# Kernel tuning notes

Measured on AMD Instinct MI355X. Metric: run time of the kernel, lower is better.

## Reference

```python
import jax, jax.numpy as jnp
import numpy as np

N_WIN = 8      # windows per side (j = i = n_win)
NUM_HEADS = 8
TOPK = 4


def setup_inputs() -> dict:
    key = jax.random.key(0)
    k1, k2 = jax.random.split(key)
    cv_feature = jax.random.normal(k1, (1, 128, 128, 256), dtype=jnp.float32)
    mv_feature = jax.random.normal(k2, (1, 4, 128, 128, 256), dtype=jnp.float32)
    return {"cv_feature": cv_feature, "mv_feature": mv_feature}


def reference(cv_feature, mv_feature):
    n, H, W, C = cv_feature.shape
    v = mv_feature.shape[1]
    j = i = N_WIN
    h, w = H // j, W // i
    p2, w2 = j * i, h * w
    m = NUM_HEADS
    ch = C // m
    scale = C ** (-0.5)  # module uses d_model**-0.5 for both routing and pixel attn

    # window partition: n (j h)(i w) c -> n (j i) h w c
    cv_patch = cv_feature.reshape(n, j, h, i, w, C).transpose(0, 1, 3, 2, 4, 5).reshape(n, p2, h, w, C)
    mv_patch = mv_feature.reshape(n, v, j, h, i, w, C).transpose(0, 1, 2, 4, 3, 5, 6).reshape(n, v, p2, h, w, C)

    q_pix = cv_patch.reshape(n, p2, w2, C)          # n p2 w2 c
    kv_pix = mv_patch.reshape(n, v, p2, w2, C)      # n v p2 w2 c

    # window-level pooled queries/keys (routing is detached in the original)
    q_win = jax.lax.stop_gradient(cv_patch.mean((2, 3)))            # n p2 c
    k_win = jax.lax.stop_gradient(mv_patch.mean((3, 4)))            # n v p2 c
    k_win = k_win.reshape(n, v * p2, C)

    logits = jnp.einsum('npc,nqc->npq', q_win * scale, k_win)       # n p2 (v p2)
    topk_logit, r_idx = jax.lax.top_k(logits, TOPK)                 # n p2 k
    r_weight = jax.nn.softmax(topk_logit, axis=-1)                  # computed, unused (faithful)

    # gather routed KV windows: n p2 k w2 c
    kv_flat = kv_pix.reshape(n, v * p2, w2, C)
    kv_sel = jnp.take_along_axis(kv_flat[:, None], r_idx[:, :, :, None, None], axis=2)

    # split heads
    k_sel = kv_sel.reshape(n, p2, TOPK, w2, m, ch)                  # n p2 k w2 m ch
    q = q_pix.reshape(n, p2, w2, m, ch)                             # n p2 w2 m ch

    attn = jnp.einsum('npqmc,npkwmc->npmqkw', q * scale, k_sel)
    attn = attn.reshape(n, p2, m, w2, TOPK * w2)
    attn = jax.nn.softmax(attn, axis=-1)

    v_sel = k_sel.transpose(0, 1, 4, 2, 3, 5).reshape(n, p2, m, TOPK * w2, ch)
    out = jnp.einsum('npmqt,npmtc->npmqc', attn, v_sel)             # n p2 m w2 ch

    # merge heads + window un-partition: -> n H W C
    out = out.transpose(0, 1, 3, 2, 4).reshape(n, j, i, h, w, C)
    out = out.transpose(0, 1, 3, 2, 4, 5).reshape(n, H, W, C)
    return out
```

## Files before the change

kernel.cpp:

```cpp
#include <hip/hip_runtime.h>
#include <hip/hip_bf16.h>


typedef __attribute__((ext_vector_type(4))) float f32x4;
typedef __attribute__((ext_vector_type(8))) short s16x8;
typedef __attribute__((ext_vector_type(4))) short s16x4;
typedef __attribute__((ext_vector_type(2))) unsigned u32x2;
typedef __attribute__((ext_vector_type(4))) unsigned u32x4;

#define SCALE 0.0625f
#define LOG2E 1.44269504088896340736f

__device__ inline unsigned cvt_pk_bf16(float lo, float hi) {
  unsigned r;
  asm("v_cvt_pk_bf16_f32 %0, %1, %2" : "=v"(r) : "v"(lo), "v"(hi));
  return r;
}
__device__ inline unsigned pk_bf16_rne(float lo, float hi) {
  unsigned a = __float_as_uint(lo);
  unsigned b = __float_as_uint(hi);
  a += 0x7FFFu + ((a >> 16) & 1u);
  b += 0x7FFFu + ((b >> 16) & 1u);
  return (a >> 16) | (b & 0xFFFF0000u);
}
#if __has_builtin(__builtin_amdgcn_exp2f)
#define EXP2(x) __builtin_amdgcn_exp2f(x)
#else
#define EXP2(x) exp2f(x)
#endif

__global__ __launch_bounds__(256) void k_means(const float* __restrict__ cv,
                                               const float* __restrict__ mv,
                                               float* __restrict__ qwin,
                                               float* __restrict__ kwin) {
  __shared__ float sm[4][64];
  int wi = blockIdx.x >> 2, cq = blockIdx.x & 3;
  int pq = threadIdx.x >> 6, cl = threadIdx.x & 63;
  int c = cq * 64 + cl;
  const float* base;
  float* dst;
  if (wi < 64) {
    base = cv + ((size_t)((wi >> 3) * 16) * 128 + (wi & 7) * 16) * 256;
    dst = qwin + wi * 256;
  } else {
    int r = wi - 64;
    base = mv + (size_t)(r >> 6) * (128 * 128 * 256)
         + ((size_t)(((r >> 3) & 7) * 16) * 128 + (r & 7) * 16) * 256;
    dst = kwin + r * 256;
  }
  float s = 0.f;
  for (int k = 0; k < 64; ++k) {
    int px = pq * 64 + k;
    s += base[((px >> 4) * 128 + (px & 15)) * 256 + c];
  }
  sm[pq][cl] = s;
  __syncthreads();
  if (pq == 0)
    dst[c] = (sm[0][cl] + sm[1][cl] + sm[2][cl] + sm[3][cl]) * (1.f / 256.f);
}

__global__ __launch_bounds__(256) void k_route(const float* __restrict__ qwin,
                                               const float* __restrict__ kwin,
                                               int* __restrict__ ridx) {
  __shared__ float qrow[256];
  __shared__ float sv[256];
  __shared__ float wbv[4];
  __shared__ int wbi[4];
  int p = blockIdx.x, t = threadIdx.x;
  qrow[t] = qwin[p * 256 + t] * SCALE;
  __syncthreads();
  const f32x4* kr = reinterpret_cast<const f32x4*>(kwin + t * 256);
  float dot = 0.f;
#pragma unroll 4
  for (int c4 = 0; c4 < 64; ++c4) {
    f32x4 kv = kr[c4];
    dot += qrow[c4 * 4 + 0] * kv[0] + qrow[c4 * 4 + 1] * kv[1]
         + qrow[c4 * 4 + 2] * kv[2] + qrow[c4 * 4 + 3] * kv[3];
  }
  sv[t] = dot;
  __syncthreads();
  for (int k = 0; k < 4; ++k) {
    float v = sv[t];
    int ii = t;
#pragma unroll
    for (int off = 32; off > 0; off >>= 1) {
      float ov = __shfl_down(v, off, 64);
      int oi = __shfl_down(ii, off, 64);
      if (ov > v || (ov == v && oi < ii)) { v = ov; ii = oi; }
    }
    if ((t & 63) == 0) { wbv[t >> 6] = v; wbi[t >> 6] = ii; }
    __syncthreads();
    if (t == 0) {
      float bv = wbv[0]; int bi = wbi[0];
      for (int j = 1; j < 4; ++j)
        if (wbv[j] > bv || (wbv[j] == bv && wbi[j] < bi)) { bv = wbv[j]; bi = wbi[j]; }
      ridx[p * 4 + k] = bi;
      sv[bi] = -3.0e38f;
    }
    __syncthreads();
  }
}

__global__ __launch_bounds__(256, 2) void k_attn(const float* __restrict__ cv,
                                                 const float* __restrict__ mv,
                                                 const int* __restrict__ ridx,
                                                 float* __restrict__ out) {
  __shared__ __align__(16) short kv_lds[256 * 32];

  const int tid = threadIdx.x;
  const int lane = tid & 63, wv = tid >> 6;
  const int g = lane >> 4, c16 = lane & 15;
  const int p = blockIdx.x >> 3, m = blockIdx.x & 7;
  const int py = p >> 3, px = p & 7;

  const int4 ridx4 = *reinterpret_cast<const int4*>(ridx + p * 4);

  const float qs = SCALE * LOG2E;
  s16x8 qf[4];
#pragma unroll
  for (int qt = 0; qt < 4; ++qt) {
    const float* qp = cv + ((size_t)((py * 16 + wv * 4 + qt) * 128) + px * 16 + c16) * 256
                         + m * 32 + g * 8;
    f32x4 a = *reinterpret_cast<const f32x4*>(qp);
    f32x4 b = *reinterpret_cast<const f32x4*>(qp + 4);
    union { u32x4 u; s16x8 s; } cu;
    cu.u[0] = cvt_pk_bf16(a[0] * qs, a[1] * qs);
    cu.u[1] = cvt_pk_bf16(a[2] * qs, a[3] * qs);
    cu.u[2] = cvt_pk_bf16(b[0] * qs, b[1] * qs);
    cu.u[3] = cvt_pk_bf16(b[2] * qs, b[3] * qs);
    qf[qt] = cu.s;
  }

  f32x4 accO[4][2];
  float lsum[4];
#pragma unroll
  for (int qt = 0; qt < 4; ++qt) {
    lsum[qt] = 0.f;
    accO[qt][0] = f32x4{0.f, 0.f, 0.f, 0.f};
    accO[qt][1] = f32x4{0.f, 0.f, 0.f, 0.f};
  }
  const f32x4 zf = {0.f, 0.f, 0.f, 0.f};

  for (int w = 0; w < 4; ++w) {
    if (w) __syncthreads();
    {
      int r = (&ridx4.x)[w];
      const float* srcb = mv + (size_t)(r >> 6) * (128 * 128 * 256)
                        + ((size_t)(((r >> 3) & 7) * 16) * 128 + (r & 7) * 16) * 256 + m * 32;
#pragma unroll
      for (int i = 0; i < 8; ++i) {
        int u = i * 256 + tid;
        int pxl = u >> 3, quad = u & 7;
        f32x4 d = *reinterpret_cast<const f32x4*>(
            srcb + ((pxl >> 4) * 128 + (pxl & 15)) * 256 + quad * 4);
        u32x2 pk;
        pk[0] = cvt_pk_bf16(d[0], d[1]);
        pk[1] = cvt_pk_bf16(d[2], d[3]);
        int off = (pxl >> 2) * 128 + (quad >> 2) * 64 + (pxl & 3) * 16 + (quad & 3) * 4;
        *reinterpret_cast<u32x2*>(&kv_lds[off]) = pk;
      }
    }
    __syncthreads();

    for (int s = 0; s < 8; ++s) {
      int kr0 = s * 32 + c16;
      int kr1 = kr0 + 16;
      const s16x8 kf0 = *reinterpret_cast<const s16x8*>(
          &kv_lds[(kr0 >> 2) * 128 + (g >> 1) * 64 + (kr0 & 3) * 16 + (g & 1) * 8]);
      const s16x8 kf1 = *reinterpret_cast<const s16x8*>(
          &kv_lds[(kr1 >> 2) * 128 + (g >> 1) * 64 + (kr1 & 3) * 16 + (g & 1) * 8]);
      s16x8 V0, V1;
#pragma unroll
      for (int j = 0; j < 8; ++j) {
        int a = (s * 8 + (j >> 2) * 4 + g) * 128 + (j & 3) * 16 + c16;
        V0[j] = kv_lds[a];
        V1[j] = kv_lds[a + 64];
      }
#pragma unroll
      for (int qt = 0; qt < 4; ++qt) {
        f32x4 sx = __builtin_amdgcn_mfma_f32_16x16x32_bf16(kf0, qf[qt], zf, 0, 0, 0);
        f32x4 sy = __builtin_amdgcn_mfma_f32_16x16x32_bf16(kf1, qf[qt], zf, 0, 0, 0);
        float x0 = EXP2(sx[0]), x1 = EXP2(sx[1]), x2 = EXP2(sx[2]), x3 = EXP2(sx[3]);
        float y0 = EXP2(sy[0]), y1 = EXP2(sy[1]), y2 = EXP2(sy[2]), y3 = EXP2(sy[3]);
        lsum[qt] += ((x0 + x1) + (x2 + x3)) + ((y0 + y1) + (y2 + y3));
        union { u32x4 u; s16x8 s; } pb;
        pb.u[0] = pk_bf16_rne(x0, x1);
        pb.u[1] = pk_bf16_rne(x2, x3);
        pb.u[2] = pk_bf16_rne(y0, y1);
        pb.u[3] = pk_bf16_rne(y2, y3);
        accO[qt][0] = __builtin_amdgcn_mfma_f32_16x16x32_bf16(V0, pb.s, accO[qt][0], 0, 0, 0);
        accO[qt][1] = __builtin_amdgcn_mfma_f32_16x16x32_bf16(V1, pb.s, accO[qt][1], 0, 0, 0);
      }
    }
  }

#pragma unroll
  for (int qt = 0; qt < 4; ++qt) {
    float l = lsum[qt];
    l += __shfl_xor(l, 16, 64);
    l += __shfl_xor(l, 32, 64);
    float rl = 1.f / l;
#pragma unroll
    for (int mt = 0; mt < 2; ++mt) {
      f32x4 o = accO[qt][mt];
      o[0] *= rl; o[1] *= rl; o[2] *= rl; o[3] *= rl;
      float* op = out + ((size_t)((py * 16 + wv * 4 + qt) * 128) + px * 16 + c16) * 256
                      + m * 32 + mt * 16 + g * 4;
      *reinterpret_cast<f32x4*>(op) = o;
    }
  }
}

extern "C" void kernel_launch(void* const* d_in, const int* in_sizes, int n_in,
                              void* d_out, int out_size, void* d_ws, size_t ws_size,
                              hipStream_t stream) {
  const float* cv = (const float*)d_in[0];
  const float* mv = (const float*)d_in[1];
  float* out = (float*)d_out;

  float* qwin = (float*)d_ws;
  float* kwin = qwin + 64 * 256;
  int* ridx = (int*)(kwin + 256 * 256);

  k_means<<<1280, 256, 0, stream>>>(cv, mv, qwin, kwin);
  k_route<<<64, 256, 0, stream>>>(qwin, kwin, ridx);
  k_attn<<<512, 256, 0, stream>>>(cv, mv, ridx, out);
}
```

Measured before the change: 71.77 us.

## Split attention over routed windows into two partial blocks plus merge kernel

Attention over the four routed KV windows is split across two blocks, each handling two windows, which doubles the grid to 1024 blocks and raises occupancy. Each block writes unnormalised partial outputs and row sums to workspace, and a new merge kernel adds the halves and normalises. This is meant to raise parallelism and latency hiding on a 256-CU device. In exchange it adds roughly 32MB of fp32 partial-output traffic plus an extra launch. If the workspace is too small it falls back to the fused kernel.

Measured after the change: 80.04 us. 11.5% more time.

```diff
diff --git a/kernel.cpp b/kernel.cpp
--- a/kernel.cpp
+++ b/kernel.cpp
@@ -4,7 +4,6 @@
 
 typedef __attribute__((ext_vector_type(4))) float f32x4;
 typedef __attribute__((ext_vector_type(8))) short s16x8;
-typedef __attribute__((ext_vector_type(4))) short s16x4;
 typedef __attribute__((ext_vector_type(2))) unsigned u32x2;
 typedef __attribute__((ext_vector_type(4))) unsigned u32x4;
 
@@ -101,19 +100,16 @@
   }
 }
 
-__global__ __launch_bounds__(256, 2) void k_attn(const float* __restrict__ cv,
-                                                 const float* __restrict__ mv,
-                                                 const int* __restrict__ ridx,
-                                                 float* __restrict__ out) {
-  __shared__ __align__(16) short kv_lds[256 * 32];
-
-  const int tid = threadIdx.x;
-  const int lane = tid & 63, wv = tid >> 6;
+template <int NW>
+__device__ __forceinline__ void attn_core(const float* __restrict__ cv,
+                                          const float* __restrict__ mv,
+                                          const int* __restrict__ rwin,
+                                          short* kv_lds,
+                                          int p, int m, int wv, int lane,
+                                          f32x4 accO[4][2], float lsum[4]) {
   const int g = lane >> 4, c16 = lane & 15;
-  const int p = blockIdx.x >> 3, m = blockIdx.x & 7;
   const int py = p >> 3, px = p & 7;
-
-  const int4 ridx4 = *reinterpret_cast<const int4*>(ridx + p * 4);
+  const int tid = wv * 64 + lane;
 
   const float qs = SCALE * LOG2E;
   s16x8 qf[4];
@@ -131,8 +127,6 @@
     qf[qt] = cu.s;
   }
 
-  f32x4 accO[4][2];
-  float lsum[4];
 #pragma unroll
   for (int qt = 0; qt < 4; ++qt) {
     lsum[qt] = 0.f;
@@ -141,10 +135,10 @@
   }
   const f32x4 zf = {0.f, 0.f, 0.f, 0.f};
 
-  for (int w = 0; w < 4; ++w) {
+  for (int w = 0; w < NW; ++w) {
     if (w) __syncthreads();
     {
-      int r = (&ridx4.x)[w];
+      int r = rwin[w];
       const float* srcb = mv + (size_t)(r >> 6) * (128 * 128 * 256)
                         + ((size_t)(((r >> 3) & 7) * 16) * 128 + (r & 7) * 16) * 256 + m * 32;
 #pragma unroll
@@ -193,6 +187,82 @@
       }
     }
   }
+}
+
+__global__ __launch_bounds__(256, 4) void k_attn_partial(const float* __restrict__ cv,
+                                                         const float* __restrict__ mv,
+                                                         const int* __restrict__ ridx,
+                                                         float* __restrict__ opart,
+                                                         float* __restrict__ lpart) {
+  __shared__ __align__(16) short kv_lds[256 * 32];
+  const int tid = threadIdx.x;
+  const int lane = tid & 63, wv = tid >> 6;
+  const int g = lane >> 4, c16 = lane & 15;
+  const int bid = blockIdx.x;
+  const int half = bid & 1, m = (bid >> 1) & 7, p = bid >> 4;
+
+  int rwin[2];
+  rwin[0] = ridx[p * 4 + half * 2 + 0];
+  rwin[1] = ridx[p * 4 + half * 2 + 1];
+
+  f32x4 accO[4][2];
+  float lsum[4];
+  attn_core<2>(cv, mv, rwin, kv_lds, p, m, wv, lane, accO, lsum);
+
+  float* Ob = opart + ((size_t)(half * 512 + p * 8 + m) * 256) * 32;
+  float* lb = lpart + (size_t)(half * 512 + p * 8 + m) * 256;
+#pragma unroll
+  for (int qt = 0; qt < 4; ++qt) {
+    float l = lsum[qt];
+    l += __shfl_xor(l, 16, 64);
+    l += __shfl_xor(l, 32, 64);
+    int q = (wv * 4 + qt) * 16 + c16;
+    if (g == 0) lb[q] = l;
+#pragma unroll
+    for (int mt = 0; mt < 2; ++mt)
+      *reinterpret_cast<f32x4*>(&Ob[q * 32 + mt * 16 + g * 4]) = accO[qt][mt];
+  }
+}
+
+__global__ __launch_bounds__(256) void k_merge(const float* __restrict__ opart,
+                                               const float* __restrict__ lpart,
+                                               float* __restrict__ out) {
+  int uidx = blockIdx.x * 256 + threadIdx.x;
+  int c4 = uidx & 63;
+  int X = (uidx >> 6) & 127;
+  int Y = uidx >> 13;
+  int p = (Y >> 4) * 8 + (X >> 4);
+  int q = (Y & 15) * 16 + (X & 15);
+  int m = c4 >> 3, ch4 = c4 & 7;
+  size_t pidx = (size_t)(p * 8 + m) * 256 + q;
+  const size_t HSTRIDE = (size_t)512 * 256;
+  f32x4 o0 = *reinterpret_cast<const f32x4*>(&opart[pidx * 32 + ch4 * 4]);
+  f32x4 o1 = *reinterpret_cast<const f32x4*>(&opart[(pidx + HSTRIDE) * 32 + ch4 * 4]);
+  float rl = 1.f / (lpart[pidx] + lpart[pidx + HSTRIDE]);
+  f32x4 o;
+  o[0] = (o0[0] + o1[0]) * rl; o[1] = (o0[1] + o1[1]) * rl;
+  o[2] = (o0[2] + o1[2]) * rl; o[3] = (o0[3] + o1[3]) * rl;
+  *reinterpret_cast<f32x4*>(&out[(size_t)uidx * 4]) = o;
+}
+
+__global__ __launch_bounds__(256, 2) void k_attn_fused(const float* __restrict__ cv,
+                                                       const float* __restrict__ mv,
+                                                       const int* __restrict__ ridx,
+                                                       float* __restrict__ out) {
+  __shared__ __align__(16) short kv_lds[256 * 32];
+  const int tid = threadIdx.x;
+  const int lane = tid & 63, wv = tid >> 6;
+  const int g = lane >> 4, c16 = lane & 15;
+  const int p = blockIdx.x >> 3, m = blockIdx.x & 7;
+  const int py = p >> 3, px = p & 7;
+
+  int rwin[4];
+#pragma unroll
+  for (int w = 0; w < 4; ++w) rwin[w] = ridx[p * 4 + w];
+
+  f32x4 accO[4][2];
+  float lsum[4];
+  attn_core<4>(cv, mv, rwin, kv_lds, p, m, wv, lane, accO, lsum);
 
 #pragma unroll
   for (int qt = 0; qt < 4; ++qt) {
@@ -219,10 +289,18 @@
   float* out = (float*)d_out;
 
   float* qwin = (float*)d_ws;
-  float* kwin = qwin + 64 * 256;
-  int* ridx = (int*)(kwin + 256 * 256);
+  float* kwin = qwin + 16384;
+  int* ridx = (int*)(kwin + 65536);
+  float* lpart = (float*)((char*)d_ws + (512u << 10));
+  float* opart = (float*)((char*)d_ws + (2u << 20));
+  const size_t WS_NEED = (2ull << 20) + 2ull * 512 * 256 * 32 * 4;
 
   k_means<<<1280, 256, 0, stream>>>(cv, mv, qwin, kwin);
   k_route<<<64, 256, 0, stream>>>(qwin, kwin, ridx);
-  k_attn<<<512, 256, 0, stream>>>(cv, mv, ridx, out);
-}
+  if (ws_size >= WS_NEED) {
+    k_attn_partial<<<1024, 256, 0, stream>>>(cv, mv, ridx, opart, lpart);
+    k_merge<<<4096, 256, 0, stream>>>(opart, lpart, out);
+  } else {
+    k_attn_fused<<<512, 256, 0, stream>>>(cv, mv, ridx, out);
+  }
+}
```
